# Kernel tuning notes

Measured on AMD Instinct MI355X. Metric: run time of the kernel, lower is better.

Reference implementation:

```python
import jax, jax.numpy as jnp
import numpy as np
from itertools import combinations

# Static conv hyperparameters (match init_kwargs)
KH = KW = 3
SH = SW = 1
PH = PW = 1
DH = DW = 1
MAJ_DIM = 3  # = kernel_size[0]


def _maj_sim(x):
    """Vectorized bipolar majority-gate simulation. x: [B, n] -> [B].
    result = sum over majority subsets of prod((1+x)_in, (1-x)_out) / 2^(n-1) - 1
    """
    n = x.shape[1]
    thresh = (n + 1) // 2
    one_plus = 1.0 + x
    one_minus = 1.0 - x
    res = jnp.zeros(x.shape[0], dtype=x.dtype)
    for k in range(thresh, n + 1):
        for combo in combinations(range(n), k):
            mask = np.zeros(n, dtype=bool)
            mask[list(combo)] = True
            res = res + jnp.prod(jnp.where(jnp.asarray(mask), one_plus, one_minus), axis=1)
    return res / (2.0 ** (n - 1)) - 1.0


def _stack_maj_sim(x, maj_dim):
    """Stacked majority tree reduction along dim 1. x: [B, n] -> [B, n_final]."""
    B = x.shape[0]
    while x.shape[1] >= maj_dim:
        num_chunks = x.shape[1] // maj_dim
        if num_chunks == 0:
            break
        z = x[:, : num_chunks * maj_dim].reshape(B * num_chunks, maj_dim)
        x = _maj_sim(z).reshape(B, num_chunks)
    return x


def _unfold(x):
    """torch.nn.functional.unfold equivalent. x:[N,C,H,W] -> [N, C*KH*KW, L].
    Feature ordering matches torch: c-major, then kernel row, then kernel col."""
    N, C, H, W = x.shape
    H_out = (H + 2 * PH - DH * (KH - 1) - 1) // SH + 1
    W_out = (W + 2 * PW - DW * (KW - 1) - 1) // SW + 1
    xp = jnp.pad(x, ((0, 0), (0, 0), (PH, PH), (PW, PW)))
    slabs = [
        xp[:, :, i * DH : i * DH + SH * (H_out - 1) + 1 : SH,
              j * DW : j * DW + SW * (W_out - 1) + 1 : SW]
        for i in range(KH) for j in range(KW)
    ]
    p = jnp.stack(slabs, axis=2)  # [N, C, KH*KW, H_out, W_out]
    return p.reshape(N, C * KH * KW, H_out * W_out)


def setup_inputs() -> dict:
    key = jax.random.key(0)
    k1, k2 = jax.random.split(key)
    x = jax.random.normal(k1, (2, 27, 64, 64), dtype=jnp.float32)
    # kaiming-uniform-ish scale for fan_in = 27*3*3 = 243
    weight = jax.random.normal(k2, (32, 27, 3, 3), dtype=jnp.float32) * 0.06
    return {"x": x, "weight": weight}


def reference(x, weight):
    N, C, H, W = x.shape
    OC = weight.shape[0]
    H_out = (H + 2 * PH - DH * (KH - 1) - 1) // SH + 1
    W_out = (W + 2 * PW - DW * (KW - 1) - 1) // SW + 1
    patches = _unfold(x)                       # [N, F, L], F = C*KH*KW
    weight_flat = weight.reshape(OC, -1)       # [OC, F]
    # prod: [N, OC, F, L]
    prod = patches[:, None, :, :] * weight_flat[None, :, :, None]
    F_ = prod.shape[2]
    L = prod.shape[3]
    # reduce the feature dim via stacked majority simulation
    z = prod.transpose(0, 1, 3, 2).reshape(N * OC * L, F_)
    out = _stack_maj_sim(z, MAJ_DIM)           # [N*OC*L, 1]
    return out.reshape(N, OC, H_out, W_out)
```

## Files before the change

### kernel.cpp

```cpp
#include <hip/hip_runtime.h>

#define CIN 27
#define HH 64
#define WW 64
#define OC 32
#define TW 16
#define TH 16
#define RS 20
#define CS (18 * RS)
#define WS 12

__device__ __forceinline__ float maj3(float a, float b, float c) {
    float s = a + b + c;
    return 0.5f * fmaf(-(a * b), c, s);
}

__device__ __forceinline__ float2 pk_maj3(float2 a, float2 b, float2 c) {
    float2 r;
    r.x = maj3(a.x, b.x, c.x);
    r.y = maj3(a.y, b.y, c.y);
    return r;
}

__global__ __launch_bounds__(128) void sconv_maj_kernel(
    const float* __restrict__ x,
    const float* __restrict__ wgt,
    float* __restrict__ out)
{
    __shared__ __align__(16) float sw[CIN * WS];
    __shared__ __align__(16) float sx[CIN * CS];

    const int tx = threadIdx.x;
    const int ty = threadIdx.y;
    const int tid = ty * 8 + tx;
    const int tile_w0 = blockIdx.x * TW;
    const int tile_h0 = blockIdx.y * TH;
    const int n  = blockIdx.z >> 5;
    const int oc = blockIdx.z & 31;

    for (int i = tid; i < CIN * 9; i += 128) {
        int c = i / 9;
        int k = i - 9 * c;
        sw[c * WS + k] = wgt[oc * (CIN * 9) + i];
    }

    const float* xn = x + (size_t)n * (CIN * HH * WW);
    for (int pos = tid; pos < 18 * 18; pos += 128) {
        int r   = pos / 18;
        int col = pos - 18 * r;
        int gr = tile_h0 + r - 1;
        int gc = tile_w0 + col - 1;
        bool ok = ((unsigned)gr < (unsigned)HH) & ((unsigned)gc < (unsigned)WW);
        int off = ok ? (gr * WW + gc) : 0;
        float* lp = sx + r * RS + col;
        #pragma unroll
        for (int c = 0; c < CIN; ++c) {
            float raw = xn[(size_t)c * (HH * WW) + off];
            lp[c * CS] = ok ? raw : 0.0f;
        }
    }
    __syncthreads();

    float2 m4[3];
    #pragma unroll
    for (int q = 0; q < 3; ++q) {
        float2 m3[3];
        #pragma unroll
        for (int t = 0; t < 3; ++t) {
            float2 m2[3];
            #pragma unroll
            for (int u = 0; u < 3; ++u) {
                const int c = q * 9 + t * 3 + u;
                float4 wa = *(const float4*)&sw[c * WS];
                float4 wb = *(const float4*)&sw[c * WS + 4];
                float  w8 = sw[c * WS + 8];
                const float wk[9] = {wa.x, wa.y, wa.z, wa.w,
                                     wb.x, wb.y, wb.z, wb.w, w8};
                float2 m1[3];
                #pragma unroll
                for (int ki = 0; ki < 3; ++ki) {
                    const float2* prow =
                        (const float2*)&sx[c * CS + (ty + ki) * RS + 2 * tx];
                    float2 v01 = prow[0];
                    float2 v23 = prow[1];
                    float w0 = wk[ki * 3 + 0];
                    float w1 = wk[ki * 3 + 1];
                    float w2 = wk[ki * 3 + 2];
                    float2 p0 = make_float2(v01.x * w0, v01.y * w0);
                    float2 p1 = make_float2(v01.y * w1, v23.x * w1);
                    float2 p2 = make_float2(v23.x * w2, v23.y * w2);
                    m1[ki] = pk_maj3(p0, p1, p2);
                }
                m2[u] = pk_maj3(m1[0], m1[1], m1[2]);
            }
            m3[t] = pk_maj3(m2[0], m2[1], m2[2]);
        }
        m4[q] = pk_maj3(m3[0], m3[1], m3[2]);
    }
    float2 res = pk_maj3(m4[0], m4[1], m4[2]);

    const int h = tile_h0 + ty;
    const int w = tile_w0 + 2 * tx;
    float2* po = (float2*)(out + (((size_t)n * OC + oc) * HH + h) * WW + w);
    *po = res;
}

extern "C" void kernel_launch(void* const* d_in, const int* in_sizes, int n_in,
                              void* d_out, int out_size, void* d_ws, size_t ws_size,
                              hipStream_t stream) {
    const float* x   = (const float*)d_in[0];
    const float* wgt = (const float*)d_in[1];
    float* out = (float*)d_out;

    dim3 block(8, 16, 1);
    dim3 grid(WW / TW, HH / TH, 2 * OC);
    sconv_maj_kernel<<<grid, block, 0, stream>>>(x, wgt, out);
}
```

Measured before the change: 70.23 us.

## Split channel groups across blocks and combine partial majority results in second kernel

The 27-channel majority tree is split into three independent 9-channel subtrees, each computed by its own block, which triples the grid and cuts shared memory per block to a third. Partial results go to a workspace buffer, and a second elementwise kernel applies the final 3-input majority. Weights are now read straight from global memory instead of being staged in shared memory. This raises parallelism and occupancy. In exchange it adds a second kernel launch, a workspace write and reread, and three times as many halo loads.

```diff
diff --git a/kernel.cpp b/kernel.cpp
--- a/kernel.cpp
+++ b/kernel.cpp
@@ -8,7 +8,7 @@
 #define TH 16
 #define RS 20
 #define CS (18 * RS)
-#define WS 12
+#define GC 9
 
 __device__ __forceinline__ float maj3(float a, float b, float c) {
     float s = a + b + c;
@@ -22,29 +22,25 @@
     return r;
 }
 
-__global__ __launch_bounds__(128) void sconv_maj_kernel(
+__global__ __launch_bounds__(128, 6) void sconv_partial_kernel(
     const float* __restrict__ x,
     const float* __restrict__ wgt,
-    float* __restrict__ out)
+    float* __restrict__ part)
 {
-    __shared__ __align__(16) float sw[CIN * WS];
-    __shared__ __align__(16) float sx[CIN * CS];
+    __shared__ __align__(16) float sx[GC * CS];
 
     const int tx = threadIdx.x;
     const int ty = threadIdx.y;
     const int tid = ty * 8 + tx;
     const int tile_w0 = blockIdx.x * TW;
     const int tile_h0 = blockIdx.y * TH;
-    const int n  = blockIdx.z >> 5;
-    const int oc = blockIdx.z & 31;
+    const int z  = blockIdx.z;
+    const int q  = z >> 6;
+    const int n  = (z >> 5) & 1;
+    const int oc = z & 31;
+    const int c0 = q * GC;
 
-    for (int i = tid; i < CIN * 9; i += 128) {
-        int c = i / 9;
-        int k = i - 9 * c;
-        sw[c * WS + k] = wgt[oc * (CIN * 9) + i];
-    }
-
-    const float* xn = x + (size_t)n * (CIN * HH * WW);
+    const float* xn = x + ((size_t)n * CIN + c0) * (HH * WW);
     for (int pos = tid; pos < 18 * 18; pos += 128) {
         int r   = pos / 18;
         int col = pos - 18 * r;
@@ -54,55 +50,71 @@
         int off = ok ? (gr * WW + gc) : 0;
         float* lp = sx + r * RS + col;
         #pragma unroll
-        for (int c = 0; c < CIN; ++c) {
+        for (int c = 0; c < GC; ++c) {
             float raw = xn[(size_t)c * (HH * WW) + off];
             lp[c * CS] = ok ? raw : 0.0f;
         }
     }
     __syncthreads();
 
-    float2 m4[3];
+    const float* wp = wgt + ((size_t)oc * CIN + c0) * 9;
+
+    float2 m3[3];
     #pragma unroll
-    for (int q = 0; q < 3; ++q) {
-        float2 m3[3];
+    for (int t = 0; t < 3; ++t) {
+        float2 m2[3];
         #pragma unroll
-        for (int t = 0; t < 3; ++t) {
-            float2 m2[3];
+        for (int u = 0; u < 3; ++u) {
+            const int c = t * 3 + u;
+            float wk[9];
             #pragma unroll
-            for (int u = 0; u < 3; ++u) {
-                const int c = q * 9 + t * 3 + u;
-                float4 wa = *(const float4*)&sw[c * WS];
-                float4 wb = *(const float4*)&sw[c * WS + 4];
-                float  w8 = sw[c * WS + 8];
-                const float wk[9] = {wa.x, wa.y, wa.z, wa.w,
-                                     wb.x, wb.y, wb.z, wb.w, w8};
-                float2 m1[3];
-                #pragma unroll
-                for (int ki = 0; ki < 3; ++ki) {
-                    const float2* prow =
-                        (const float2*)&sx[c * CS + (ty + ki) * RS + 2 * tx];
-                    float2 v01 = prow[0];
-                    float2 v23 = prow[1];
-                    float w0 = wk[ki * 3 + 0];
-                    float w1 = wk[ki * 3 + 1];
-                    float w2 = wk[ki * 3 + 2];
-                    float2 p0 = make_float2(v01.x * w0, v01.y * w0);
-                    float2 p1 = make_float2(v01.y * w1, v23.x * w1);
-                    float2 p2 = make_float2(v23.x * w2, v23.y * w2);
-                    m1[ki] = pk_maj3(p0, p1, p2);
-                }
-                m2[u] = pk_maj3(m1[0], m1[1], m1[2]);
+            for (int k = 0; k < 9; ++k) wk[k] = wp[c * 9 + k];
+            float2 m1[3];
+            #pragma unroll
+            for (int ki = 0; ki < 3; ++ki) {
+                const float2* prow =
+                    (const float2*)&sx[c * CS + (ty + ki) * RS + 2 * tx];
+                float2 v01 = prow[0];
+                float2 v23 = prow[1];
+                float w0 = wk[ki * 3 + 0];
+                float w1 = wk[ki * 3 + 1];
+                float w2 = wk[ki * 3 + 2];
+                float2 p0 = make_float2(v01.x * w0, v01.y * w0);
+                float2 p1 = make_float2(v01.y * w1, v23.x * w1);
+                float2 p2 = make_float2(v23.x * w2, v23.y * w2);
+                m1[ki] = pk_maj3(p0, p1, p2);
             }
-            m3[t] = pk_maj3(m2[0], m2[1], m2[2]);
+            m2[u] = pk_maj3(m1[0], m1[1], m1[2]);
         }
-        m4[q] = pk_maj3(m3[0], m3[1], m3[2]);
+        m3[t] = pk_maj3(m2[0], m2[1], m2[2]);
     }
-    float2 res = pk_maj3(m4[0], m4[1], m4[2]);
+    float2 m4 = pk_maj3(m3[0], m3[1], m3[2]);
 
     const int h = tile_h0 + ty;
     const int w = tile_w0 + 2 * tx;
-    float2* po = (float2*)(out + (((size_t)n * OC + oc) * HH + h) * WW + w);
-    *po = res;
+    float2* po = (float2*)(part + ((((size_t)q * 2 + n) * OC + oc) * HH + h) * WW + w);
+    *po = m4;
+}
+
+#define NPIX (2 * OC * HH * WW)
+
+__global__ __launch_bounds__(256) void sconv_combine_kernel(
+    const float* __restrict__ part,
+    float* __restrict__ out)
+{
+    int i = blockIdx.x * 256 + threadIdx.x;
+    const float4* p0 = (const float4*)part;
+    const float4* p1 = (const float4*)(part + NPIX);
+    const float4* p2 = (const float4*)(part + 2 * NPIX);
+    float4 a = p0[i];
+    float4 b = p1[i];
+    float4 c = p2[i];
+    float4 r;
+    r.x = maj3(a.x, b.x, c.x);
+    r.y = maj3(a.y, b.y, c.y);
+    r.z = maj3(a.z, b.z, c.z);
+    r.w = maj3(a.w, b.w, c.w);
+    ((float4*)out)[i] = r;
 }
 
 extern "C" void kernel_launch(void* const* d_in, const int* in_sizes, int n_in,
@@ -110,9 +122,14 @@
                               hipStream_t stream) {
     const float* x   = (const float*)d_in[0];
     const float* wgt = (const float*)d_in[1];
-    float* out = (float*)d_out;
+    float* out  = (float*)d_out;
+    float* part = (float*)d_ws;
 
     dim3 block(8, 16, 1);
-    dim3 grid(WW / TW, HH / TH, 2 * OC);
-    sconv_maj_kernel<<<grid, block, 0, stream>>>(x, wgt, out);
+    dim3 grid(WW / TW, HH / TH, 3 * 2 * OC);
+    sconv_partial_kernel<<<grid, block, 0, stream>>>(x, wgt, part);
+
+    dim3 cblock(256, 1, 1);
+    dim3 cgrid(NPIX / 4 / 256, 1, 1);
+    sconv_combine_kernel<<<cgrid, cblock, 0, stream>>>(part, out);
 }
```

Result: no change. 69.41 us (-1.2%).

## Split channel groups across threadIdx.z and give each thread four output pixels

Applied to the files above, without the earlier changes.

The block grows from 128 to 192 threads laid out 4x16x3. Each z-slice reduces one group of 9 channels through the first majority tree levels for four adjacent output pixels, reusing a float4+float2 row load. The three partial results are then combined through shared memory after an extra barrier, and the q==0 slice writes float4 outputs. This gives more threads per tile to share the staging load and more register-level reuse of input rows, at the cost of two extra syncs and idle threads in the final combine.

```diff
diff --git a/kernel.cpp b/kernel.cpp
--- a/kernel.cpp
+++ b/kernel.cpp
@@ -15,14 +15,7 @@
     return 0.5f * fmaf(-(a * b), c, s);
 }
 
-__device__ __forceinline__ float2 pk_maj3(float2 a, float2 b, float2 c) {
-    float2 r;
-    r.x = maj3(a.x, b.x, c.x);
-    r.y = maj3(a.y, b.y, c.y);
-    return r;
-}
-
-__global__ __launch_bounds__(128) void sconv_maj_kernel(
+__global__ __launch_bounds__(192, 3) void sconv_maj_kernel(
     const float* __restrict__ x,
     const float* __restrict__ wgt,
     float* __restrict__ out)
@@ -32,20 +25,21 @@
 
     const int tx = threadIdx.x;
     const int ty = threadIdx.y;
-    const int tid = ty * 8 + tx;
+    const int q  = threadIdx.z;
+    const int tid = tx + 4 * (ty + 16 * q);
     const int tile_w0 = blockIdx.x * TW;
     const int tile_h0 = blockIdx.y * TH;
     const int n  = blockIdx.z >> 5;
     const int oc = blockIdx.z & 31;
 
-    for (int i = tid; i < CIN * 9; i += 128) {
+    for (int i = tid; i < CIN * 9; i += 192) {
         int c = i / 9;
         int k = i - 9 * c;
         sw[c * WS + k] = wgt[oc * (CIN * 9) + i];
     }
 
     const float* xn = x + (size_t)n * (CIN * HH * WW);
-    for (int pos = tid; pos < 18 * 18; pos += 128) {
+    for (int pos = tid; pos < 18 * 18; pos += 192) {
         int r   = pos / 18;
         int col = pos - 18 * r;
         int gr = tile_h0 + r - 1;
@@ -61,48 +55,67 @@
     }
     __syncthreads();
 
-    float2 m4[3];
+    const int c0 = q * 9;
+    float m3_[3][4];
     #pragma unroll
-    for (int q = 0; q < 3; ++q) {
-        float2 m3[3];
+    for (int t = 0; t < 3; ++t) {
+        float m2_[3][4];
         #pragma unroll
-        for (int t = 0; t < 3; ++t) {
-            float2 m2[3];
+        for (int u = 0; u < 3; ++u) {
+            const int c = c0 + t * 3 + u;
+            float4 wa = *(const float4*)&sw[c * WS];
+            float4 wb = *(const float4*)&sw[c * WS + 4];
+            float  w8 = sw[c * WS + 8];
+            const float wk[9] = {wa.x, wa.y, wa.z, wa.w,
+                                 wb.x, wb.y, wb.z, wb.w, w8};
+            float m1_[3][4];
             #pragma unroll
-            for (int u = 0; u < 3; ++u) {
-                const int c = q * 9 + t * 3 + u;
-                float4 wa = *(const float4*)&sw[c * WS];
-                float4 wb = *(const float4*)&sw[c * WS + 4];
-                float  w8 = sw[c * WS + 8];
-                const float wk[9] = {wa.x, wa.y, wa.z, wa.w,
-                                     wb.x, wb.y, wb.z, wb.w, w8};
-                float2 m1[3];
+            for (int ki = 0; ki < 3; ++ki) {
+                const float* prow = &sx[c * CS + (ty + ki) * RS + 4 * tx];
+                float4 v4 = *(const float4*)prow;
+                float2 v2 = *(const float2*)(prow + 4);
+                const float in6[6] = {v4.x, v4.y, v4.z, v4.w, v2.x, v2.y};
+                float w0 = wk[ki * 3 + 0];
+                float w1 = wk[ki * 3 + 1];
+                float w2 = wk[ki * 3 + 2];
                 #pragma unroll
-                for (int ki = 0; ki < 3; ++ki) {
-                    const float2* prow =
-                        (const float2*)&sx[c * CS + (ty + ki) * RS + 2 * tx];
-                    float2 v01 = prow[0];
-                    float2 v23 = prow[1];
-                    float w0 = wk[ki * 3 + 0];
-                    float w1 = wk[ki * 3 + 1];
-                    float w2 = wk[ki * 3 + 2];
-                    float2 p0 = make_float2(v01.x * w0, v01.y * w0);
-                    float2 p1 = make_float2(v01.y * w1, v23.x * w1);
-                    float2 p2 = make_float2(v23.x * w2, v23.y * w2);
-                    m1[ki] = pk_maj3(p0, p1, p2);
+                for (int j = 0; j < 4; ++j) {
+                    m1_[ki][j] = maj3(in6[j] * w0, in6[j + 1] * w1, in6[j + 2] * w2);
                 }
-                m2[u] = pk_maj3(m1[0], m1[1], m1[2]);
             }
-            m3[t] = pk_maj3(m2[0], m2[1], m2[2]);
+            #pragma unroll
+            for (int j = 0; j < 4; ++j)
+                m2_[u][j] = maj3(m1_[0][j], m1_[1][j], m1_[2][j]);
         }
-        m4[q] = pk_maj3(m3[0], m3[1], m3[2]);
+        #pragma unroll
+        for (int j = 0; j < 4; ++j)
+            m3_[t][j] = maj3(m2_[0][j], m2_[1][j], m2_[2][j]);
     }
-    float2 res = pk_maj3(m4[0], m4[1], m4[2]);
+    float m4_[4];
+    #pragma unroll
+    for (int j = 0; j < 4; ++j)
+        m4_[j] = maj3(m3_[0][j], m3_[1][j], m3_[2][j]);
 
-    const int h = tile_h0 + ty;
-    const int w = tile_w0 + 2 * tx;
-    float2* po = (float2*)(out + (((size_t)n * OC + oc) * HH + h) * WW + w);
-    *po = res;
+    __syncthreads();
+    float* sp = sx;
+    const int px = ty * TW + 4 * tx;
+    if (q > 0)
+        *(float4*)&sp[(q - 1) * 256 + px] =
+            make_float4(m4_[0], m4_[1], m4_[2], m4_[3]);
+    __syncthreads();
+
+    if (q == 0) {
+        float4 b = *(const float4*)&sp[px];
+        float4 c = *(const float4*)&sp[256 + px];
+        float4 r;
+        r.x = maj3(m4_[0], b.x, c.x);
+        r.y = maj3(m4_[1], b.y, c.y);
+        r.z = maj3(m4_[2], b.z, c.z);
+        r.w = maj3(m4_[3], b.w, c.w);
+        const int h = tile_h0 + ty;
+        const int w = tile_w0 + 4 * tx;
+        *(float4*)(out + (((size_t)n * OC + oc) * HH + h) * WW + w) = r;
+    }
 }
 
 extern "C" void kernel_launch(void* const* d_in, const int* in_sizes, int n_in,
@@ -112,7 +125,7 @@
     const float* wgt = (const float*)d_in[1];
     float* out = (float*)d_out;
 
-    dim3 block(8, 16, 1);
+    dim3 block(4, 16, 3);
     dim3 grid(WW / TW, HH / TH, 2 * OC);
     sconv_maj_kernel<<<grid, block, 0, stream>>>(x, wgt, out);
 }
```

Result: faster. 68.68 us (-2.2%).
